# Performance work log

Hardware: AMD Instinct MI355X
Metric: run time of the kernel (lower is better)

## Reference

```python
import jax, jax.numpy as jnp
import numpy as np

B, N, DIM = 4, 8192, 512
HEADS, DHEAD = 8, 64
INNER = HEADS * DHEAD          # 512
M = 256                        # num landmarks
L = N // M                     # tokens per landmark group (n % m == 0 -> no pad)
ITERS = 6                      # Moore-Penrose iterations
KRES = 33                      # residual depthwise conv kernel (along n)
SCALE = DHEAD ** -0.5


def setup_inputs() -> dict:
    key = jax.random.key(0)
    k1, k2, k3, k4 = jax.random.split(key, 4)
    return {
        "x": jax.random.normal(k1, (B, N, DIM), jnp.float32),
        "w_qkv": jax.random.normal(k2, (DIM, 3 * INNER), jnp.float32) * (DIM ** -0.5),
        "w_out": jax.random.normal(k3, (INNER, DIM), jnp.float32) * (INNER ** -0.5),
        "b_out": jnp.zeros((DIM,), jnp.float32),
        "res_kernel": jax.random.normal(k4, (HEADS, 1, KRES, 1), jnp.float32) * 0.05,
    }


def _moore_penrose_pinv(x, iters=ITERS):
    # x: (b, h, m, m)
    abs_x = jnp.abs(x)
    col = abs_x.sum(axis=-1)
    row = abs_x.sum(axis=-2)
    z = jnp.swapaxes(x, -1, -2) / (jnp.max(col) * jnp.max(row))
    I = jnp.eye(x.shape[-1], dtype=x.dtype)
    for _ in range(iters):
        xz = x @ z
        z = 0.25 * z @ (13 * I - xz @ (15 * I - xz @ (7 * I - xz)))
    return z


def reference(x, w_qkv, w_out, b_out, res_kernel):
    b, n, _ = x.shape
    qkv = x @ w_qkv                               # (b, n, 3*inner)
    q, k, v = jnp.split(qkv, 3, axis=-1)
    to_heads = lambda t: t.reshape(b, n, HEADS, DHEAD).transpose(0, 2, 1, 3)  # (b,h,n,d)
    q, k, v = to_heads(q), to_heads(k), to_heads(v)
    q = q * SCALE

    # landmarks: mean over consecutive groups of L tokens -> (b,h,M,d)
    q_l = q.reshape(b, HEADS, M, L, DHEAD).sum(axis=3) / L
    k_l = k.reshape(b, HEADS, M, L, DHEAD).sum(axis=3) / L

    attn1 = jax.nn.softmax(jnp.einsum('bhid,bhjd->bhij', q, k_l), axis=-1)    # (b,h,n,M)
    attn2 = jax.nn.softmax(jnp.einsum('bhid,bhjd->bhij', q_l, k_l), axis=-1)  # (b,h,M,M)
    attn3 = jax.nn.softmax(jnp.einsum('bhid,bhjd->bhij', q_l, k), axis=-1)    # (b,h,M,n)

    out = attn1 @ _moore_penrose_pinv(attn2) @ (attn3 @ v)                    # (b,h,n,d)

    # depthwise residual conv over the sequence axis, per head
    res = jax.lax.conv_general_dilated(
        v, res_kernel, window_strides=(1, 1),
        padding=[(KRES // 2, KRES // 2), (0, 0)],
        dimension_numbers=('NCHW', 'OIHW', 'NCHW'),
        feature_group_count=HEADS)
    out = out + res

    out = out.transpose(0, 2, 1, 3).reshape(b, n, INNER)
    return out @ w_out + b_out
```

## Files before the change

### kernel.cpp

```cpp
#include <hip/hip_runtime.h>
#include <stdint.h>
#include <stddef.h>


typedef __bf16 bf16x8 __attribute__((ext_vector_type(8)));
typedef __bf16 bf16x4 __attribute__((ext_vector_type(4)));
typedef float f32x4 __attribute__((ext_vector_type(4)));

__device__ __forceinline__ f32x4 mfma_bf16(bf16x8 a, bf16x8 b, f32x4 c) {
    return __builtin_amdgcn_mfma_f32_16x16x32_bf16(a, b, c, 0, 0, 0);
}

__device__ __forceinline__ void gload16(const __bf16* g, __bf16* l) {
    __builtin_amdgcn_global_load_lds(
        (const __attribute__((address_space(1))) void*)g,
        (__attribute__((address_space(3))) void*)l, 16, 0, 0);
}

__global__ void k_init_stats(float* stats) { stats[0] = 1.f; stats[1] = 0.f; }

__global__ __launch_bounds__(256) void k_cvt(const float* __restrict__ in,
        __bf16* __restrict__ out) {
    size_t base = ((size_t)blockIdx.x * 256 + threadIdx.x) * 8;
    float4 a = *(const float4*)&in[base];
    float4 b = *(const float4*)&in[base + 4];
    bf16x8 o;
    o[0] = (__bf16)a.x; o[1] = (__bf16)a.y; o[2] = (__bf16)a.z; o[3] = (__bf16)a.w;
    o[4] = (__bf16)b.x; o[5] = (__bf16)b.y; o[6] = (__bf16)b.z; o[7] = (__bf16)b.w;
    *(bf16x8*)&out[base] = o;
}

__global__ __launch_bounds__(256) void k_transpose_f32(const float* __restrict__ in,
        __bf16* __restrict__ out, int R, int C) {
    __shared__ __bf16 tile[64 * 72];
    int r0 = blockIdx.x * 64, c0 = blockIdx.y * 64;
    int tid = threadIdx.x;
    #pragma unroll
    for (int i = 0; i < 16; ++i) {
        int slot = i * 256 + tid;
        int rr = slot >> 6, cc = slot & 63;
        tile[rr * 72 + cc] = (__bf16)in[(size_t)(r0 + rr) * C + c0 + cc];
    }
    __syncthreads();
    #pragma unroll
    for (int i = 0; i < 2; ++i) {
        int slot = i * 256 + tid;
        int cc = slot >> 3, s = slot & 7;
        bf16x8 t;
        #pragma unroll
        for (int j = 0; j < 8; ++j) t[j] = tile[(s * 8 + j) * 72 + cc];
        *(bf16x8*)&out[(size_t)(c0 + cc) * R + r0 + s * 8] = t;
    }
}

__global__ __launch_bounds__(256) void k_transpose_bf(const __bf16* __restrict__ in,
        __bf16* __restrict__ out, int R, int C, long bsi, long bso) {
    __shared__ __bf16 tile[64 * 72];
    in  += (size_t)blockIdx.z * bsi;
    out += (size_t)blockIdx.z * bso;
    int r0 = blockIdx.x * 64, c0 = blockIdx.y * 64;
    int tid = threadIdx.x;
    #pragma unroll
    for (int i = 0; i < 2; ++i) {
        int slot = i * 256 + tid;
        int rr = slot >> 3, s = slot & 7;
        *(bf16x8*)&tile[rr * 72 + s * 8] =
            *(const bf16x8*)&in[(size_t)(r0 + rr) * C + c0 + s * 8];
    }
    __syncthreads();
    #pragma unroll
    for (int i = 0; i < 2; ++i) {
        int slot = i * 256 + tid;
        int cc = slot >> 3, s = slot & 7;
        bf16x8 t;
        #pragma unroll
        for (int j = 0; j < 8; ++j) t[j] = tile[(s * 8 + j) * 72 + cc];
        *(bf16x8*)&out[(size_t)(c0 + cc) * R + r0 + s * 8] = t;
    }
}

template<int MODE>
__global__ __launch_bounds__(256) void k_gemm_big(const __bf16* __restrict__ A,
        const __bf16* __restrict__ Bt, int K,
        __bf16* __restrict__ qp, __bf16* __restrict__ kp, __bf16* __restrict__ vp,
        float* __restrict__ outp, const float* __restrict__ bias) {
    __shared__ __bf16 sA[128 * 64];
    __shared__ __bf16 sB[128 * 64];
    constexpr int NT  = (MODE == 0) ? 12 : 4;
    constexpr int TOT = (MODE == 0) ? 3072 : 1024;
    int flat = blockIdx.x;
    int t = (flat & 7) * (TOT / 8) + (flat >> 3);
    int m0 = (t / NT) * 128, n0 = (t % NT) * 128;
    int tid = threadIdx.x;
    int wave = tid >> 6, l = tid & 63, lm = l & 15, lq = l >> 4;
    int wm = wave & 1, wn = wave >> 1;
    int lr = l >> 3, lc8 = l & 7;
    int src_c = (lc8 ^ lr) * 8;
    f32x4 acc[4][4] = {};
    for (int k0 = 0; k0 < K; k0 += 64) {
        #pragma unroll
        for (int i = 0; i < 4; ++i) {
            int g = wave * 4 + i;
            gload16(&A[(size_t)(m0 + g * 8 + lr) * K + k0 + src_c], &sA[g * 512]);
        }
        #pragma unroll
        for (int i = 0; i < 4; ++i) {
            int g = wave * 4 + i;
            gload16(&Bt[(size_t)(n0 + g * 8 + lr) * K + k0 + src_c], &sB[g * 512]);
        }
        __syncthreads();
        #pragma unroll
        for (int ko = 0; ko < 2; ++ko) {
            int ch = (ko << 2) | lq;
            bf16x8 af[4], bfr[4];
            #pragma unroll
            for (int mi = 0; mi < 4; ++mi) {
                int r = wm * 64 + mi * 16 + lm;
                af[mi] = *(bf16x8*)&sA[r * 64 + ((ch ^ (r & 7)) << 3)];
            }
            #pragma unroll
            for (int ni = 0; ni < 4; ++ni) {
                int r = wn * 64 + ni * 16 + lm;
                bfr[ni] = *(bf16x8*)&sB[r * 64 + ((ch ^ (r & 7)) << 3)];
            }
            #pragma unroll
            for (int mi = 0; mi < 4; ++mi)
                #pragma unroll
                for (int ni = 0; ni < 4; ++ni)
                    acc[mi][ni] = mfma_bf16(af[mi], bfr[ni], acc[mi][ni]);
        }
        __syncthreads();
    }
    #pragma unroll
    for (int mi = 0; mi < 4; ++mi)
    #pragma unroll
    for (int ni = 0; ni < 4; ++ni)
    #pragma unroll
    for (int reg = 0; reg < 4; ++reg) {
        int gr = m0 + wm * 64 + mi * 16 + lq * 4 + reg;
        int gc = n0 + wn * 64 + ni * 16 + lm;
        float v = acc[mi][ni][reg];
        if (MODE == 0) {
            int which = gc >> 9, rem = gc & 511;
            int h = rem >> 6, d = rem & 63;
            int b = gr >> 13, tok = gr & 8191;
            size_t dst = ((size_t)((b * 8 + h) * 8192 + tok)) * 64 + d;
            if (which == 0)      qp[dst] = (__bf16)(v * 0.125f);
            else if (which == 1) kp[dst] = (__bf16)v;
            else                 vp[dst] = (__bf16)v;
        } else {
            outp[(size_t)gr * 512 + gc] = v + bias[gc];
        }
    }
}

__global__ __launch_bounds__(256) void k_landmarks(const __bf16* __restrict__ q,
        const __bf16* __restrict__ k, __bf16* __restrict__ ql, __bf16* __restrict__ kl) {
    int idx = blockIdx.x * 256 + threadIdx.x;
    int sel = idx >> 19;
    int rem = idx & 524287;
    int bh = rem >> 14;
    int m  = (rem >> 6) & 255;
    int d  = rem & 63;
    const __bf16* src = sel ? k : q;
    __bf16* dst = sel ? kl : ql;
    const __bf16* p = src + ((size_t)(bh * 8192 + m * 32)) * 64 + d;
    float s = 0.f;
    #pragma unroll
    for (int j = 0; j < 32; ++j) s += (float)p[j * 64];
    dst[(size_t)bh * 16384 + m * 64 + d] = (__bf16)(s * (1.f / 32.f));
}

__global__ __launch_bounds__(256) void k_attn2(const __bf16* __restrict__ ql,
        const __bf16* __restrict__ kl, __bf16* __restrict__ ph, __bf16* __restrict__ pl) {
    int tid = threadIdx.x;
    int wave = tid >> 6, l = tid & 63, lm = l & 15, lq = l >> 4;
    int bh = blockIdx.y;
    int r0 = blockIdx.x * 64 + wave * 16;
    const __bf16* qb = ql + (size_t)bh * 16384;
    const __bf16* kb = kl + (size_t)bh * 16384;
    bf16x8 af[2];
    #pragma unroll
    for (int ko = 0; ko < 2; ++ko)
        af[ko] = *(const bf16x8*)&qb[(size_t)(r0 + lm) * 64 + ko * 32 + lq * 8];
    f32x4 S[16] = {};
    #pragma unroll
    for (int ci = 0; ci < 16; ++ci)
        #pragma unroll
        for (int ko = 0; ko < 2; ++ko) {
            bf16x8 bfr = *(const bf16x8*)&kb[(size_t)(ci * 16 + lm) * 64 + ko * 32 + lq * 8];
            S[ci] = mfma_bf16(af[ko], bfr, S[ci]);
        }
    __bf16* oh = ph + (size_t)bh * 65536;
    __bf16* ol = pl + (size_t)bh * 65536;
    #pragma unroll
    for (int reg = 0; reg < 4; ++reg) {
        float sum = 0.f;
        #pragma unroll
        for (int ci = 0; ci < 16; ++ci) {
            float e = __expf(S[ci][reg]); S[ci][reg] = e; sum += e;
        }
        #pragma unroll
        for (int msk = 1; msk < 16; msk <<= 1) sum += __shfl_xor(sum, msk);
        float inv = 1.f / sum;
        int row = r0 + lq * 4 + reg;
        #pragma unroll
        for (int ci = 0; ci < 16; ++ci) {
            float v = S[ci][reg] * inv;
            __bf16 hh = (__bf16)v;
            oh[(size_t)row * 256 + ci * 16 + lm] = hh;
            ol[(size_t)row * 256 + ci * 16 + lm] = (__bf16)(v - (float)hh);
        }
    }
}

__global__ __launch_bounds__(256) void k_stats(const __bf16* __restrict__ ph,
        const __bf16* __restrict__ pl, float* stats) {
    __shared__ float red[256];
    int tid = threadIdx.x;
    const __bf16* a = ph + (size_t)blockIdx.x * 65536;
    const __bf16* b = pl + (size_t)blockIdx.x * 65536;
    float cs = 0.f;
    for (int r = 0; r < 256; ++r)
        cs += (float)a[r * 256 + tid] + (float)b[r * 256 + tid];
    red[tid] = cs; __syncthreads();
    for (int off = 128; off > 0; off >>= 1) {
        if (tid < off) red[tid] = fmaxf(red[tid], red[tid + off]);
        __syncthreads();
    }
    if (tid == 0) atomicMax((int*)&stats[1], __float_as_int(red[0]));
}

__global__ __launch_bounds__(256) void k_z0(const __bf16* __restrict__ ph,
        const __bf16* __restrict__ pl, const float* __restrict__ stats,
        __bf16* __restrict__ zh, __bf16* __restrict__ zl) {
    int idx = blockIdx.x * 256 + threadIdx.x;
    int bh = idx >> 16, r = (idx >> 8) & 255, c = idx & 255;
    float inv = 1.f / (stats[0] * stats[1]);
    size_t src = ((size_t)bh << 16) + (size_t)c * 256 + r;
    float v = ((float)ph[src] + (float)pl[src]) * inv;
    __bf16 hh = (__bf16)v;
    zh[idx] = hh;
    zl[idx] = (__bf16)(v - (float)hh);
}

__device__ __forceinline__ void pgemm_core(const __bf16* __restrict__ Ah,
        const __bf16* __restrict__ Al, const __bf16* __restrict__ Bth,
        const __bf16* __restrict__ Btl, int m0, int n0,
        __bf16* sAh, __bf16* sAl, __bf16* sBh, __bf16* sBl, f32x4 acc[2][2]) {
    int tid = threadIdx.x;
    int wave = tid >> 6, l = tid & 63, lm = l & 15, lq = l >> 4;
    int wm = wave & 1, wn = wave >> 1;
    int lr = l >> 3, lc8 = l & 7;
    int src_c = (lc8 ^ lr) * 8;
    for (int k0 = 0; k0 < 256; k0 += 64) {
        #pragma unroll
        for (int i = 0; i < 2; ++i) {
            int g = wave * 2 + i;
            size_t ra = (size_t)(m0 + g * 8 + lr) * 256 + k0 + src_c;
            size_t rb = (size_t)(n0 + g * 8 + lr) * 256 + k0 + src_c;
            gload16(&Ah[ra], &sAh[g * 512]);
            gload16(&Al[ra], &sAl[g * 512]);
            gload16(&Bth[rb], &sBh[g * 512]);
            gload16(&Btl[rb], &sBl[g * 512]);
        }
        __syncthreads();
        #pragma unroll
        for (int ko = 0; ko < 2; ++ko) {
            int ch = (ko << 2) | lq;
            bf16x8 ah[2], al2[2], bh2[2], bl2[2];
            #pragma unroll
            for (int mi = 0; mi < 2; ++mi) {
                int r = wm * 32 + mi * 16 + lm;
                int o = r * 64 + ((ch ^ (r & 7)) << 3);
                ah[mi]  = *(bf16x8*)&sAh[o];
                al2[mi] = *(bf16x8*)&sAl[o];
            }
            #pragma unroll
            for (int ni = 0; ni < 2; ++ni) {
                int r = wn * 32 + ni * 16 + lm;
                int o = r * 64 + ((ch ^ (r & 7)) << 3);
                bh2[ni] = *(bf16x8*)&sBh[o];
                bl2[ni] = *(bf16x8*)&sBl[o];
            }
            #pragma unroll
            for (int mi = 0; mi < 2; ++mi)
                #pragma unroll
                for (int ni = 0; ni < 2; ++ni) {
                    acc[mi][ni] = mfma_bf16(ah[mi], bh2[ni], acc[mi][ni]);
                    acc[mi][ni] = mfma_bf16(ah[mi], bl2[ni], acc[mi][ni]);
                    acc[mi][ni] = mfma_bf16(al2[mi], bh2[ni], acc[mi][ni]);
                }
        }
        __syncthreads();
    }
}

__global__ __launch_bounds__(256) void k_pgemm(const __bf16* __restrict__ Ah,
        const __bf16* __restrict__ Al, const __bf16* __restrict__ Bth,
        const __bf16* __restrict__ Btl, const __bf16* __restrict__ Ch,
        const __bf16* __restrict__ Cl, __bf16* __restrict__ OutH,
        __bf16* __restrict__ OutL, float alpha, const float* __restrict__ sPtr,
        float beta, float delta, int outMode, long bStride) {
    __shared__ __bf16 sAh[64 * 64], sAl[64 * 64], sBh[64 * 64], sBl[64 * 64];
    int tid = threadIdx.x;
    int wave = tid >> 6, l = tid & 63, lm = l & 15, lq = l >> 4;
    int wm = wave & 1, wn = wave >> 1;
    int bh = blockIdx.z;
    int m0 = blockIdx.x * 64, n0 = blockIdx.y * 64;
    float aEff = alpha;
    if (sPtr) aEff *= 1.f / (sPtr[0] * sPtr[1]);
    f32x4 acc[2][2] = {};
    pgemm_core(Ah + (size_t)bh * 65536, Al + (size_t)bh * 65536,
               Bth + (size_t)bh * bStride, Btl + (size_t)bh * bStride,
               m0, n0, sAh, sAl, sBh, sBl, acc);
    #pragma unroll
    for (int mi = 0; mi < 2; ++mi)
    #pragma unroll
    for (int ni = 0; ni < 2; ++ni)
    #pragma unroll
    for (int reg = 0; reg < 4; ++reg) {
        int gr = m0 + wm * 32 + mi * 16 + lq * 4 + reg;
        int gc = n0 + wn * 32 + ni * 16 + lm;
        float v = aEff * acc[mi][ni][reg];
        if (beta != 0.f) {
            size_t ci = (size_t)bh * 65536 + (size_t)gr * 256 + gc;
            v += beta * ((float)Ch[ci] + (float)Cl[ci]);
        }
        if (gr == gc) v += delta;
        if (outMode == 0) {
            size_t di = (size_t)bh * 65536 + (size_t)gr * 256 + gc;
            __bf16 hh = (__bf16)v;
            OutH[di] = hh;
            OutL[di] = (__bf16)(v - (float)hh);
        } else {
            int ci2 = gr >> 4, lqm = (gr >> 2) & 3, r = gr & 3;
            int slot = ((ci2 >> 1) << 5) + (lqm << 3) + ((ci2 & 1) << 2) + r;
            OutH[(size_t)bh * 16384 + (size_t)gc * 256 + slot] = (__bf16)v;
        }
    }
}

__global__ __launch_bounds__(256) void k_pgemm_dual(const __bf16* __restrict__ Zh,
        const __bf16* __restrict__ Zl, const __bf16* __restrict__ A2h,
        const __bf16* __restrict__ A2l, const __bf16* __restrict__ Bth,
        const __bf16* __restrict__ Btl, __bf16* __restrict__ OzH,
        __bf16* __restrict__ OzL, __bf16* __restrict__ OaH, __bf16* __restrict__ OaL) {
    __shared__ __bf16 sAh[64 * 64], sAl[64 * 64], sBh[64 * 64], sBl[64 * 64];
    int tid = threadIdx.x;
    int wave = tid >> 6, l = tid & 63, lm = l & 15, lq = l >> 4;
    int wm = wave & 1, wn = wave >> 1;
    int zz = blockIdx.z, bh = zz & 31;
    const __bf16* Lh = (zz >= 32 ? A2h : Zh) + (size_t)bh * 65536;
    const __bf16* Ll = (zz >= 32 ? A2l : Zl) + (size_t)bh * 65536;
    __bf16* Oh = (zz >= 32 ? OaH : OzH) + (size_t)bh * 65536;
    __bf16* Ol = (zz >= 32 ? OaL : OzL) + (size_t)bh * 65536;
    int m0 = blockIdx.x * 64, n0 = blockIdx.y * 64;
    f32x4 acc[2][2] = {};
    pgemm_core(Lh, Ll, Bth + (size_t)bh * 65536, Btl + (size_t)bh * 65536,
               m0, n0, sAh, sAl, sBh, sBl, acc);
    #pragma unroll
    for (int mi = 0; mi < 2; ++mi)
    #pragma unroll
    for (int ni = 0; ni < 2; ++ni)
    #pragma unroll
    for (int reg = 0; reg < 4; ++reg) {
        int gr = m0 + wm * 32 + mi * 16 + lq * 4 + reg;
        int gc = n0 + wn * 32 + ni * 16 + lm;
        float v = 0.25f * acc[mi][ni][reg];
        __bf16 hh = (__bf16)v;
        Oh[(size_t)gr * 256 + gc] = hh;
        Ol[(size_t)gr * 256 + gc] = (__bf16)(v - (float)hh);
    }
}

__global__ __launch_bounds__(256) void k_attn3(const __bf16* __restrict__ ql,
        const __bf16* __restrict__ kk, const __bf16* __restrict__ vt,
        float* __restrict__ O_s, float* __restrict__ l_s) {
    int tid = threadIdx.x;
    int wave = tid >> 6, l = tid & 63, lm = l & 15, lq = l >> 4;
    int s = blockIdx.x, bh = blockIdx.y;
    const __bf16* qb = ql + (size_t)bh * 16384;
    bf16x8 qa[4][2];
    #pragma unroll
    for (int mi = 0; mi < 4; ++mi)
        #pragma unroll
        for (int ko = 0; ko < 2; ++ko)
            qa[mi][ko] = *(const bf16x8*)&qb[(size_t)(wave * 64 + mi * 16 + lm) * 64 + ko * 32 + lq * 8];
    f32x4 O[4][4] = {};
    float lsum[4] = {};
    for (int it = 0; it < 8; ++it) {
        int c0 = s * 512 + it * 64;
        bf16x8 kf[4][2];
        #pragma unroll
        for (int ci = 0; ci < 4; ++ci)
            #pragma unroll
            for (int ko = 0; ko < 2; ++ko)
                kf[ci][ko] = *(const bf16x8*)&kk[((size_t)bh * 8192 + c0 + ci * 16 + lm) * 64 + ko * 32 + lq * 8];
        f32x4 St[4][4] = {};
        #pragma unroll
        for (int ci = 0; ci < 4; ++ci)
            #pragma unroll
            for (int ko = 0; ko < 2; ++ko)
                #pragma unroll
                for (int mi = 0; mi < 4; ++mi)
                    St[mi][ci] = mfma_bf16(kf[ci][ko], qa[mi][ko], St[mi][ci]);
        bf16x4 pk[4][4];
        #pragma unroll
        for (int mi = 0; mi < 4; ++mi)
            #pragma unroll
            for (int ci = 0; ci < 4; ++ci)
                #pragma unroll
                for (int reg = 0; reg < 4; ++reg) {
                    float e = __expf(St[mi][ci][reg]);
                    lsum[mi] += e;
                    pk[mi][ci][reg] = (__bf16)e;
                }
        #pragma unroll
        for (int ko = 0; ko < 2; ++ko) {
            bf16x8 af[4];
            #pragma unroll
            for (int mi = 0; mi < 4; ++mi)
                #pragma unroll
                for (int r = 0; r < 4; ++r) {
                    af[mi][r]     = pk[mi][2 * ko][r];
                    af[mi][4 + r] = pk[mi][2 * ko + 1][r];
                }
            #pragma unroll
            for (int ni = 0; ni < 4; ++ni) {
                const __bf16* vrow = &vt[((size_t)bh * 64 + ni * 16 + lm) * 8192 + c0 + ko * 32 + lq * 4];
                bf16x4 v0 = *(const bf16x4*)&vrow[0];
                bf16x4 v1 = *(const bf16x4*)&vrow[16];
                bf16x8 vb;
                #pragma unroll
                for (int r = 0; r < 4; ++r) { vb[r] = v0[r]; vb[4 + r] = v1[r]; }
                #pragma unroll
                for (int mi = 0; mi < 4; ++mi)
                    O[mi][ni] = mfma_bf16(af[mi], vb, O[mi][ni]);
            }
        }
    }
    #pragma unroll
    for (int mi = 0; mi < 4; ++mi) {
        float v = lsum[mi];
        v += __shfl_xor(v, 16);
        v += __shfl_xor(v, 32);
        lsum[mi] = v;
    }
    int base = (bh * 16 + s) * 256;
    #pragma unroll
    for (int mi = 0; mi < 4; ++mi)
        if (lq == 0) l_s[base + wave * 64 + mi * 16 + lm] = lsum[mi];
    #pragma unroll
    for (int mi = 0; mi < 4; ++mi)
        #pragma unroll
        for (int reg = 0; reg < 4; ++reg) {
            int r = wave * 64 + mi * 16 + lq * 4 + reg;
            #pragma unroll
            for (int ni = 0; ni < 4; ++ni)
                O_s[((size_t)(base + r)) * 64 + ni * 16 + lm] = O[mi][ni][reg];
        }
}

__global__ __launch_bounds__(256) void k_t2combine(const float* __restrict__ O_s,
        const float* __restrict__ l_s, __bf16* __restrict__ t2th,
        __bf16* __restrict__ t2tl) {
    int idx = blockIdx.x * 256 + threadIdx.x;
    int bh = idx >> 14, r = (idx >> 6) & 255, d = idx & 63;
    float den = 0.f, num = 0.f;
    #pragma unroll
    for (int s = 0; s < 16; ++s) {
        int b2 = (bh * 16 + s) * 256 + r;
        den += l_s[b2];
        num += O_s[(size_t)b2 * 64 + d];
    }
    float v = num / den;
    __bf16 hh = (__bf16)v;
    size_t di = ((size_t)bh * 64 + d) * 256 + r;
    t2th[di] = hh;
    t2tl[di] = (__bf16)(v - (float)hh);
}

__global__ __launch_bounds__(256) void k_conv(const __bf16* __restrict__ vt,
        const float* __restrict__ resk, __bf16* __restrict__ convb) {
    int bh = blockIdx.y, h = bh & 7;
    int d = threadIdx.x & 63, tg = threadIdx.x >> 6;
    int t0 = blockIdx.x * 64 + tg * 16;
    __shared__ float kfs[33];
    if (threadIdx.x < 33) kfs[threadIdx.x] = resk[h * 33 + threadIdx.x];
    __syncthreads();
    const __bf16* row = vt + ((size_t)bh * 64 + d) * 8192;
    float win[48];
    #pragma unroll
    for (int c = 0; c < 6; ++c) {
        int tok0 = t0 - 16 + c * 8;
        if (tok0 >= 0 && tok0 + 7 < 8192) {
            bf16x8 v8 = *(const bf16x8*)&row[tok0];
            #pragma unroll
            for (int e = 0; e < 8; ++e) win[c * 8 + e] = (float)v8[e];
        } else {
            #pragma unroll
            for (int e = 0; e < 8; ++e) {
                int tok = tok0 + e;
                win[c * 8 + e] = (tok >= 0 && tok < 8192) ? (float)row[tok] : 0.f;
            }
        }
    }
    float o[16];
    #pragma unroll
    for (int i = 0; i < 16; ++i) o[i] = 0.f;
    #pragma unroll
    for (int j = 0; j < 33; ++j) {
        float kf = kfs[j];
        #pragma unroll
        for (int i = 0; i < 16; ++i) o[i] += kf * win[i + j];
    }
    __bf16* outr = convb + ((size_t)bh * 8192) * 64 + d;
    #pragma unroll
    for (int i = 0; i < 16; ++i)
        outr[(size_t)(t0 + i) * 64] = (__bf16)o[i];
}

__global__ __launch_bounds__(256) void k_attn1(const __bf16* __restrict__ q,
        const __bf16* __restrict__ kl, const __bf16* __restrict__ zt2p,
        const __bf16* __restrict__ convb, __bf16* __restrict__ outp) {
    int tid = threadIdx.x;
    int wave = tid >> 6, l = tid & 63, lm = l & 15, lq = l >> 4;
    int bh = blockIdx.y;
    int t0 = blockIdx.x * 256;
    int b = bh >> 3, h = bh & 7;
    const __bf16* qb = q + (size_t)bh * 8192 * 64;
    const __bf16* kb = kl + (size_t)bh * 16384;
    const __bf16* zb = zt2p + (size_t)bh * 16384;
    int rowb = t0 + wave * 64;
    bf16x8 qa[4][2];
    #pragma unroll
    for (int mi = 0; mi < 4; ++mi)
        #pragma unroll
        for (int ko = 0; ko < 2; ++ko)
            qa[mi][ko] = *(const bf16x8*)&qb[(size_t)(rowb + mi * 16 + lm) * 64 + ko * 32 + lq * 8];
    f32x4 O[4][4] = {};
    float rs[4] = {};
    #pragma unroll
    for (int c2 = 0; c2 < 8; ++c2) {
        bf16x8 kf[2][2];
        #pragma unroll
        for (int ci = 0; ci < 2; ++ci)
            #pragma unroll
            for (int ko = 0; ko < 2; ++ko)
                kf[ci][ko] = *(const bf16x8*)&kb[(size_t)((c2 * 2 + ci) * 16 + lm) * 64 + ko * 32 + lq * 8];
        f32x4 St[4][2] = {};
        #pragma unroll
        for (int ci = 0; ci < 2; ++ci)
            #pragma unroll
            for (int ko = 0; ko < 2; ++ko)
                #pragma unroll
                for (int mi = 0; mi < 4; ++mi)
                    St[mi][ci] = mfma_bf16(kf[ci][ko], qa[mi][ko], St[mi][ci]);
        bf16x4 pk[4][2];
        #pragma unroll
        for (int mi = 0; mi < 4; ++mi)
            #pragma unroll
            for (int ci = 0; ci < 2; ++ci)
                #pragma unroll
                for (int reg = 0; reg < 4; ++reg) {
                    float e = __expf(St[mi][ci][reg]);
                    rs[mi] += e;
                    pk[mi][ci][reg] = (__bf16)e;
                }
        bf16x8 zfr[4];
        #pragma unroll
        for (int ni = 0; ni < 4; ++ni)
            zfr[ni] = *(const bf16x8*)&zb[(size_t)(ni * 16 + lm) * 256 + c2 * 32 + lq * 8];
        #pragma unroll
        for (int mi = 0; mi < 4; ++mi) {
            bf16x8 af;
            #pragma unroll
            for (int r = 0; r < 4; ++r) {
                af[r]     = pk[mi][0][r];
                af[4 + r] = pk[mi][1][r];
            }
            #pragma unroll
            for (int ni = 0; ni < 4; ++ni)
                O[mi][ni] = mfma_bf16(af, zfr[ni], O[mi][ni]);
        }
    }
    #pragma unroll
    for (int mi = 0; mi < 4; ++mi) {
        float v = rs[mi];
        v += __shfl_xor(v, 16);
        v += __shfl_xor(v, 32);
        float invr[4];
        #pragma unroll
        for (int reg = 0; reg < 4; ++reg)
            invr[reg] = 1.f / __shfl(v, lq * 4 + reg);
        #pragma unroll
        for (int ni = 0; ni < 4; ++ni)
            #pragma unroll
            for (int reg = 0; reg < 4; ++reg) {
                int tok = rowb + mi * 16 + lq * 4 + reg;
                int d = ni * 16 + lm;
                float conv = (float)convb[((size_t)bh * 8192 + tok) * 64 + d];
                float val = O[mi][ni][reg] * invr[reg] + conv;
                outp[((size_t)(b * 8192 + tok)) * 512 + h * 64 + d] = (__bf16)val;
            }
    }
}

extern "C" void kernel_launch(void* const* d_in, const int* in_sizes, int n_in,
                              void* d_out, int out_size, void* d_ws, size_t ws_size,
                              hipStream_t stream) {
    const float* x    = (const float*)d_in[0];
    const float* wqkv = (const float*)d_in[1];
    const float* wout = (const float*)d_in[2];
    const float* bout = (const float*)d_in[3];
    const float* resk = (const float*)d_in[4];
    char* ws = (char*)d_ws;
    size_t off = 0;
    auto alloc = [&](size_t bytes) {
        char* p = ws + off;
        off += (bytes + 255) & ~(size_t)255;
        return p;
    };
    const size_t PL = 2097152;
    __bf16* q_bf   = (__bf16*)alloc(33554432);
    __bf16* k_bf   = (__bf16*)alloc(33554432);
    __bf16* vt     = (__bf16*)alloc(33554432);
    __bf16* outpre = (__bf16*)alloc(33554432);
    __bf16* q_l    = (__bf16*)alloc(1048576);
    __bf16* k_l    = (__bf16*)alloc(1048576);
    __bf16* a2h    = (__bf16*)alloc(8388608);
    __bf16* zAh    = (__bf16*)alloc(8388608);
    __bf16* zBh    = (__bf16*)alloc(8388608);
    __bf16* Amh    = (__bf16*)alloc(8388608);
    __bf16* W2h    = (__bf16*)alloc(8388608);
    __bf16* W3h    = (__bf16*)alloc(8388608);
    float*  O_s    = (float*)alloc(33554432);
    float*  l_s    = (float*)alloc(524288);
    __bf16* t2th   = (__bf16*)alloc(2097152);
    __bf16* zt2t   = (__bf16*)alloc(1048576);
    __bf16* wqkvt  = (__bf16*)alloc(1572864);
    __bf16* woutt  = (__bf16*)alloc(524288);
    float*  stats  = (float*)alloc(256);
    __bf16* convb  = (__bf16*)O_s;
    __bf16* xb     = (__bf16*)O_s;
    __bf16* a2l = a2h + PL;
    __bf16* zAl = zAh + PL;
    __bf16* zBl = zBh + PL;
    __bf16* Aml = Amh + PL;
    __bf16* W2l = W2h + PL;
    __bf16* W3l = W3h + PL;
    __bf16* t2tl = t2th + 524288;

    k_init_stats<<<1, 1, 0, stream>>>(stats);
    k_cvt<<<8192, 256, 0, stream>>>(x, xb);
    k_transpose_f32<<<dim3(8, 24), 256, 0, stream>>>(wqkv, wqkvt, 512, 1536);
    k_transpose_f32<<<dim3(8, 8), 256, 0, stream>>>(wout, woutt, 512, 512);
    k_gemm_big<0><<<3072, 256, 0, stream>>>(xb, wqkvt, 512,
            q_bf, k_bf, outpre, nullptr, nullptr);
    k_transpose_bf<<<dim3(128, 1, 32), 256, 0, stream>>>(outpre, vt, 8192, 64, 524288, 524288);
    k_landmarks<<<4096, 256, 0, stream>>>(q_bf, k_bf, q_l, k_l);
    k_attn2<<<dim3(4, 32), 256, 0, stream>>>(q_l, k_l, a2h, a2l);
    k_stats<<<32, 256, 0, stream>>>(a2h, a2l, stats);
    k_z0<<<8192, 256, 0, stream>>>(a2h, a2l, stats, zAh, zAl);
    k_attn3<<<dim3(16, 32), 256, 0, stream>>>(q_l, k_bf, vt, O_s, l_s);
    k_t2combine<<<2048, 256, 0, stream>>>(O_s, l_s, t2th, t2tl);
    k_conv<<<dim3(128, 32), 256, 0, stream>>>(vt, resk, convb);
    k_pgemm<<<dim3(4, 4, 32), 256, 0, stream>>>(a2h, a2l, a2h, a2l,
            nullptr, nullptr, Amh, Aml, 1.f, stats, 0.f, 0.f, 0, 65536);
    __bf16 *zch = zAh, *zcl = zAl, *znh = zBh, *znl = zBl;
    __bf16 *Ach = Amh, *Acl = Aml, *Anh = a2h, *Anl = a2l;
    for (int it = 0; it < 6; ++it) {
        k_pgemm<<<dim3(4, 4, 32), 256, 0, stream>>>(Ach, Acl, Ach, Acl,
                Ach, Acl, W2h, W2l, 1.f, nullptr, -7.f, 15.f, 0, 65536);
        k_pgemm<<<dim3(4, 4, 32), 256, 0, stream>>>(Ach, Acl, W2h, W2l,
                nullptr, nullptr, W3h, W3l, -1.f, nullptr, 0.f, 13.f, 0, 65536);
        if (it < 5) {
            k_pgemm_dual<<<dim3(4, 4, 64), 256, 0, stream>>>(zch, zcl, Ach, Acl,
                    W3h, W3l, znh, znl, Anh, Anl);
            __bf16* t;
            t = Ach; Ach = Anh; Anh = t;
            t = Acl; Acl = Anl; Anl = t;
        } else {
            k_pgemm_dual<<<dim3(4, 4, 32), 256, 0, stream>>>(zch, zcl, zch, zcl,
                    W3h, W3l, znh, znl, znh, znl);
        }
        __bf16* t;
        t = zch; zch = znh; znh = t;
        t = zcl; zcl = znl; znl = t;
    }
    k_pgemm<<<dim3(4, 1, 32), 256, 0, stream>>>(zch, zcl, t2th, t2tl,
            nullptr, nullptr, zt2t, nullptr, 1.f, nullptr, 0.f, 0.f, 1, 16384);
    k_attn1<<<dim3(32, 32), 256, 0, stream>>>(q_bf, k_l, zt2t, convb, outpre);
    k_gemm_big<1><<<1024, 256, 0, stream>>>(outpre, woutt, 512,
            nullptr, nullptr, nullptr, (float*)d_out, bout);
}
```

Baseline: 692.7 us.

## Halve pinv GEMM tile height, swizzle block order for XCD locality, fold stats init

The batched 256x256 pinv GEMMs now use 32x64 tiles instead of 64x64, doubling the block count (512 to 1024 per launch) to fill more CUs. Blocks use a flattened 1D grid with an XCD-aware remap (flat&7 times stride) so that tiles of the same batch-head land on the same XCD and share L2. The stats init kernel is folded into the convert kernel to save one launch. Smaller tiles lower arithmetic intensity and cause more B-tile reloads per output.

```diff
diff --git a/kernel.cpp b/kernel.cpp
--- a/kernel.cpp
+++ b/kernel.cpp
@@ -17,10 +17,9 @@
         (__attribute__((address_space(3))) void*)l, 16, 0, 0);
 }
 
-__global__ void k_init_stats(float* stats) { stats[0] = 1.f; stats[1] = 0.f; }
-
 __global__ __launch_bounds__(256) void k_cvt(const float* __restrict__ in,
-        __bf16* __restrict__ out) {
+        __bf16* __restrict__ out, float* __restrict__ stats) {
+    if (blockIdx.x == 0 && threadIdx.x == 0) { stats[0] = 1.f; stats[1] = 0.f; }
     size_t base = ((size_t)blockIdx.x * 256 + threadIdx.x) * 8;
     float4 a = *(const float4*)&in[base];
     float4 b = *(const float4*)&in[base + 4];
@@ -247,20 +246,22 @@
 __device__ __forceinline__ void pgemm_core(const __bf16* __restrict__ Ah,
         const __bf16* __restrict__ Al, const __bf16* __restrict__ Bth,
         const __bf16* __restrict__ Btl, int m0, int n0,
-        __bf16* sAh, __bf16* sAl, __bf16* sBh, __bf16* sBl, f32x4 acc[2][2]) {
+        __bf16* sAh, __bf16* sAl, __bf16* sBh, __bf16* sBl, f32x4 acc[2]) {
     int tid = threadIdx.x;
     int wave = tid >> 6, l = tid & 63, lm = l & 15, lq = l >> 4;
     int wm = wave & 1, wn = wave >> 1;
     int lr = l >> 3, lc8 = l & 7;
     int src_c = (lc8 ^ lr) * 8;
     for (int k0 = 0; k0 < 256; k0 += 64) {
+        {
+            size_t ra = (size_t)(m0 + wave * 8 + lr) * 256 + k0 + src_c;
+            gload16(&Ah[ra], &sAh[wave * 512]);
+            gload16(&Al[ra], &sAl[wave * 512]);
+        }
         #pragma unroll
         for (int i = 0; i < 2; ++i) {
             int g = wave * 2 + i;
-            size_t ra = (size_t)(m0 + g * 8 + lr) * 256 + k0 + src_c;
             size_t rb = (size_t)(n0 + g * 8 + lr) * 256 + k0 + src_c;
-            gload16(&Ah[ra], &sAh[g * 512]);
-            gload16(&Al[ra], &sAl[g * 512]);
             gload16(&Bth[rb], &sBh[g * 512]);
             gload16(&Btl[rb], &sBl[g * 512]);
         }
@@ -268,29 +269,24 @@
         #pragma unroll
         for (int ko = 0; ko < 2; ++ko) {
             int ch = (ko << 2) | lq;
-            bf16x8 ah[2], al2[2], bh2[2], bl2[2];
-            #pragma unroll
-            for (int mi = 0; mi < 2; ++mi) {
-                int r = wm * 32 + mi * 16 + lm;
-                int o = r * 64 + ((ch ^ (r & 7)) << 3);
-                ah[mi]  = *(bf16x8*)&sAh[o];
-                al2[mi] = *(bf16x8*)&sAl[o];
-            }
+            int rA = wm * 16 + lm;
+            int oA = rA * 64 + ((ch ^ (rA & 7)) << 3);
+            bf16x8 a_h = *(bf16x8*)&sAh[oA];
+            bf16x8 a_l = *(bf16x8*)&sAl[oA];
+            bf16x8 b_h[2], b_l[2];
             #pragma unroll
             for (int ni = 0; ni < 2; ++ni) {
                 int r = wn * 32 + ni * 16 + lm;
                 int o = r * 64 + ((ch ^ (r & 7)) << 3);
-                bh2[ni] = *(bf16x8*)&sBh[o];
-                bl2[ni] = *(bf16x8*)&sBl[o];
-            }
-            #pragma unroll
-            for (int mi = 0; mi < 2; ++mi)
-                #pragma unroll
-                for (int ni = 0; ni < 2; ++ni) {
-                    acc[mi][ni] = mfma_bf16(ah[mi], bh2[ni], acc[mi][ni]);
-                    acc[mi][ni] = mfma_bf16(ah[mi], bl2[ni], acc[mi][ni]);
-                    acc[mi][ni] = mfma_bf16(al2[mi], bh2[ni], acc[mi][ni]);
-                }
+                b_h[ni] = *(bf16x8*)&sBh[o];
+                b_l[ni] = *(bf16x8*)&sBl[o];
+            }
+            #pragma unroll
+            for (int ni = 0; ni < 2; ++ni) {
+                acc[ni] = mfma_bf16(a_h, b_h[ni], acc[ni]);
+                acc[ni] = mfma_bf16(a_h, b_l[ni], acc[ni]);
+                acc[ni] = mfma_bf16(a_l, b_h[ni], acc[ni]);
+            }
         }
         __syncthreads();
     }
@@ -302,27 +298,30 @@
         const __bf16* __restrict__ Cl, __bf16* __restrict__ OutH,
         __bf16* __restrict__ OutL, float alpha, const float* __restrict__ sPtr,
         float beta, float delta, int outMode, long bStride) {
-    __shared__ __bf16 sAh[64 * 64], sAl[64 * 64], sBh[64 * 64], sBl[64 * 64];
+    __shared__ __bf16 sAh[32 * 64], sAl[32 * 64], sBh[64 * 64], sBl[64 * 64];
     int tid = threadIdx.x;
     int wave = tid >> 6, l = tid & 63, lm = l & 15, lq = l >> 4;
     int wm = wave & 1, wn = wave >> 1;
-    int bh = blockIdx.z;
-    int m0 = blockIdx.x * 64, n0 = blockIdx.y * 64;
+    int total = gridDim.x;
+    int flat = blockIdx.x;
+    int t = (flat & 7) * (total >> 3) + (flat >> 3);
+    int ntb = total >> 8;
+    int tpb = ntb << 3;
+    int bh = t / tpb, rem = t - bh * tpb;
+    int m0 = (rem / ntb) * 32, n0 = (rem % ntb) * 64;
     float aEff = alpha;
     if (sPtr) aEff *= 1.f / (sPtr[0] * sPtr[1]);
-    f32x4 acc[2][2] = {};
+    f32x4 acc[2] = {};
     pgemm_core(Ah + (size_t)bh * 65536, Al + (size_t)bh * 65536,
                Bth + (size_t)bh * bStride, Btl + (size_t)bh * bStride,
                m0, n0, sAh, sAl, sBh, sBl, acc);
     #pragma unroll
-    for (int mi = 0; mi < 2; ++mi)
-    #pragma unroll
     for (int ni = 0; ni < 2; ++ni)
     #pragma unroll
     for (int reg = 0; reg < 4; ++reg) {
-        int gr = m0 + wm * 32 + mi * 16 + lq * 4 + reg;
+        int gr = m0 + wm * 16 + lq * 4 + reg;
         int gc = n0 + wn * 32 + ni * 16 + lm;
-        float v = aEff * acc[mi][ni][reg];
+        float v = aEff * acc[ni][reg];
         if (beta != 0.f) {
             size_t ci = (size_t)bh * 65536 + (size_t)gr * 256 + gc;
             v += beta * ((float)Ch[ci] + (float)Cl[ci]);
@@ -346,28 +345,30 @@
         const __bf16* __restrict__ A2l, const __bf16* __restrict__ Bth,
         const __bf16* __restrict__ Btl, __bf16* __restrict__ OzH,
         __bf16* __restrict__ OzL, __bf16* __restrict__ OaH, __bf16* __restrict__ OaL) {
-    __shared__ __bf16 sAh[64 * 64], sAl[64 * 64], sBh[64 * 64], sBl[64 * 64];
+    __shared__ __bf16 sAh[32 * 64], sAl[32 * 64], sBh[64 * 64], sBl[64 * 64];
     int tid = threadIdx.x;
     int wave = tid >> 6, l = tid & 63, lm = l & 15, lq = l >> 4;
     int wm = wave & 1, wn = wave >> 1;
-    int zz = blockIdx.z, bh = zz & 31;
+    int total = gridDim.x;
+    int flat = blockIdx.x;
+    int t = (flat & 7) * (total >> 3) + (flat >> 3);
+    int zz = t >> 5, rem = t & 31;
+    int m0 = (rem >> 2) * 32, n0 = (rem & 3) * 64;
+    int bh = zz & 31;
     const __bf16* Lh = (zz >= 32 ? A2h : Zh) + (size_t)bh * 65536;
     const __bf16* Ll = (zz >= 32 ? A2l : Zl) + (size_t)bh * 65536;
     __bf16* Oh = (zz >= 32 ? OaH : OzH) + (size_t)bh * 65536;
     __bf16* Ol = (zz >= 32 ? OaL : OzL) + (size_t)bh * 65536;
-    int m0 = blockIdx.x * 64, n0 = blockIdx.y * 64;
-    f32x4 acc[2][2] = {};
+    f32x4 acc[2] = {};
     pgemm_core(Lh, Ll, Bth + (size_t)bh * 65536, Btl + (size_t)bh * 65536,
                m0, n0, sAh, sAl, sBh, sBl, acc);
     #pragma unroll
-    for (int mi = 0; mi < 2; ++mi)
-    #pragma unroll
     for (int ni = 0; ni < 2; ++ni)
     #pragma unroll
     for (int reg = 0; reg < 4; ++reg) {
-        int gr = m0 + wm * 32 + mi * 16 + lq * 4 + reg;
+        int gr = m0 + wm * 16 + lq * 4 + reg;
         int gc = n0 + wn * 32 + ni * 16 + lm;
-        float v = 0.25f * acc[mi][ni][reg];
+        float v = 0.25f * acc[ni][reg];
         __bf16 hh = (__bf16)v;
         Oh[(size_t)gr * 256 + gc] = hh;
         Ol[(size_t)gr * 256 + gc] = (__bf16)(v - (float)hh);
@@ -652,8 +653,7 @@
     __bf16* W3l = W3h + PL;
     __bf16* t2tl = t2th + 524288;
 
-    k_init_stats<<<1, 1, 0, stream>>>(stats);
-    k_cvt<<<8192, 256, 0, stream>>>(x, xb);
+    k_cvt<<<8192, 256, 0, stream>>>(x, xb, stats);
     k_transpose_f32<<<dim3(8, 24), 256, 0, stream>>>(wqkv, wqkvt, 512, 1536);
     k_transpose_f32<<<dim3(8, 8), 256, 0, stream>>>(wout, woutt, 512, 512);
     k_gemm_big<0><<<3072, 256, 0, stream>>>(xb, wqkvt, 512,
@@ -666,30 +666,30 @@
     k_attn3<<<dim3(16, 32), 256, 0, stream>>>(q_l, k_bf, vt, O_s, l_s);
     k_t2combine<<<2048, 256, 0, stream>>>(O_s, l_s, t2th, t2tl);
     k_conv<<<dim3(128, 32), 256, 0, stream>>>(vt, resk, convb);
-    k_pgemm<<<dim3(4, 4, 32), 256, 0, stream>>>(a2h, a2l, a2h, a2l,
+    k_pgemm<<<1024, 256, 0, stream>>>(a2h, a2l, a2h, a2l,
             nullptr, nullptr, Amh, Aml, 1.f, stats, 0.f, 0.f, 0, 65536);
     __bf16 *zch = zAh, *zcl = zAl, *znh = zBh, *znl = zBl;
     __bf16 *Ach = Amh, *Acl = Aml, *Anh = a2h, *Anl = a2l;
     for (int it = 0; it < 6; ++it) {
-        k_pgemm<<<dim3(4, 4, 32), 256, 0, stream>>>(Ach, Acl, Ach, Acl,
+        k_pgemm<<<1024, 256, 0, stream>>>(Ach, Acl, Ach, Acl,
                 Ach, Acl, W2h, W2l, 1.f, nullptr, -7.f, 15.f, 0, 65536);
-        k_pgemm<<<dim3(4, 4, 32), 256, 0, stream>>>(Ach, Acl, W2h, W2l,
+        k_pgemm<<<1024, 256, 0, stream>>>(Ach, Acl, W2h, W2l,
                 nullptr, nullptr, W3h, W3l, -1.f, nullptr, 0.f, 13.f, 0, 65536);
         if (it < 5) {
-            k_pgemm_dual<<<dim3(4, 4, 64), 256, 0, stream>>>(zch, zcl, Ach, Acl,
+            k_pgemm_dual<<<2048, 256, 0, stream>>>(zch, zcl, Ach, Acl,
                     W3h, W3l, znh, znl, Anh, Anl);
             __bf16* t;
             t = Ach; Ach = Anh; Anh = t;
             t = Acl; Acl = Anl; Anl = t;
         } else {
-            k_pgemm_dual<<<dim3(4, 4, 32), 256, 0, stream>>>(zch, zcl, zch, zcl,
+            k_pgemm_dual<<<1024, 256, 0, stream>>>(zch, zcl, zch, zcl,
                     W3h, W3l, znh, znl, znh, znl);
         }
         __bf16* t;
         t = zch; zch = znh; znh = t;
         t = zcl; zcl = znl; znl = t;
     }
-    k_pgemm<<<dim3(4, 1, 32), 256, 0, stream>>>(zch, zcl, t2th, t2tl,
+    k_pgemm<<<256, 256, 0, stream>>>(zch, zcl, t2th, t2tl,
             nullptr, nullptr, zt2t, nullptr, 1.f, nullptr, 0.f, 0.f, 1, 16384);
     k_attn1<<<dim3(32, 32), 256, 0, stream>>>(q_bf, k_l, zt2t, convb, outpre);
     k_gemm_big<1><<<1024, 256, 0, stream>>>(outpre, woutt, 512,
```

After: 642.0 us. -7.3%, faster.
